# Optimization experiments

Hardware: AMD Instinct MI355X
Metric: run time of the kernel (lower is better)

The kernel has to match this reference:

```python
import jax, jax.numpy as jnp
import numpy as np

N_NODES = 100000
N_EDGES = 1250000
NUM_RELS = 8
D_IN, D_HID, D_OUT = 64, 64, 32


def setup_inputs() -> dict:
    key = jax.random.key(0)
    ks = jax.random.split(key, 10)
    x = jax.random.normal(ks[0], (N_NODES, D_IN), dtype=jnp.float32)
    src = jax.random.randint(ks[1], (N_EDGES,), 0, N_NODES, dtype=jnp.int32)
    dst = jax.random.randint(ks[2], (N_EDGES,), 0, N_NODES, dtype=jnp.int32)
    edge_type = jax.random.randint(ks[3], (N_EDGES,), 0, NUM_RELS, dtype=jnp.int32)
    s1 = 1.0 / np.sqrt(D_IN)
    s2 = 1.0 / np.sqrt(D_HID)
    W1 = jax.random.uniform(ks[4], (NUM_RELS, D_IN, D_HID), jnp.float32, -s1, s1)
    root1 = jax.random.uniform(ks[5], (D_IN, D_HID), jnp.float32, -s1, s1)
    b1 = jnp.zeros((D_HID,), jnp.float32)
    W2 = jax.random.uniform(ks[6], (NUM_RELS, D_HID, D_OUT), jnp.float32, -s2, s2)
    root2 = jax.random.uniform(ks[7], (D_HID, D_OUT), jnp.float32, -s2, s2)
    b2 = jnp.zeros((D_OUT,), jnp.float32)
    return {"x": x, "W1": W1, "root1": root1, "b1": b1,
            "W2": W2, "root2": root2, "b2": b2,
            "src": src, "dst": dst, "edge_type": edge_type}


def rgcn_conv(x, W, root, b, src, dst, edge_type, num_rels, num_nodes):
    # self-loop (root) transform + bias
    out = x @ root + b
    for r in range(num_rels):  # loop over small fixed relation set
        mask = (edge_type == r).astype(x.dtype)          # (E,)
        h = x @ W[r]                                      # (N, dout): transform once per relation
        msg = h[src] * mask[:, None]                      # (E, dout) gather + mask
        agg = jax.ops.segment_sum(msg, dst, num_segments=num_nodes)
        cnt = jax.ops.segment_sum(mask, dst, num_segments=num_nodes)
        out = out + agg / jnp.maximum(cnt, 1.0)[:, None]  # per-relation mean (PyG default aggr)
    return out


def reference(x, W1, root1, b1, W2, root2, b2, src, dst, edge_type):
    h = jax.nn.relu(rgcn_conv(x, W1, root1, b1, src, dst, edge_type, NUM_RELS, N_NODES))
    return rgcn_conv(h, W2, root2, b2, src, dst, edge_type, NUM_RELS, N_NODES)
```

## Files before the change

kernel.cpp:

```cpp
#include <hip/hip_runtime.h>

typedef _Float16 half8 __attribute__((ext_vector_type(8)));
typedef __attribute__((ext_vector_type(4))) float f32x4;

__device__ __forceinline__ unsigned short f2h(float f) {
    _Float16 h = (_Float16)f;
    return *(unsigned short*)&h;
}
__device__ __forceinline__ float h2f(unsigned short u) {
    _Float16 h = *(_Float16*)&u;
    return (float)h;
}


__device__ __forceinline__ void wprep_body(
    const float* __restrict__ W, const float* __restrict__ root,
    unsigned short* __restrict__ wb, int dout, int idx)
{
    int c = idx / (64 * dout);
    int rme = idx % (64 * dout);
    int kk = rme / dout;
    int j = rme % dout;
    float f = (c == 0) ? root[kk * dout + j]
                       : W[(size_t)(c - 1) * 64 * dout + kk * dout + j];
    wb[(size_t)c * dout * 72 + (size_t)j * 72 + kk] = f2h(f);
}

__global__ __launch_bounds__(256) void prep_kernel(
    const float* __restrict__ x, unsigned short* __restrict__ xh, int n8,
    const float* __restrict__ W1, const float* __restrict__ root1,
    unsigned short* __restrict__ wb1,
    const float* __restrict__ W2, const float* __restrict__ root2,
    unsigned short* __restrict__ wb2,
    int* __restrict__ hist, int nhist4)
{
    int id = blockIdx.x * 256 + threadIdx.x;
    if (id < n8) {
        const f32x4* p = (const f32x4*)(x + (size_t)id * 8);
        f32x4 u = p[0], v = p[1];
        half8 o;
#pragma unroll
        for (int j = 0; j < 4; ++j) {
            o[j] = (_Float16)u[j];
            o[j + 4] = (_Float16)v[j];
        }
        *(half8*)(xh + (size_t)id * 8) = o;
        return;
    }
    id -= n8;
    if (id < 9 * 64 * 64) { wprep_body(W1, root1, wb1, 64, id); return; }
    id -= 9 * 64 * 64;
    if (id < 9 * 64 * 32) { wprep_body(W2, root2, wb2, 32, id); return; }
    id -= 9 * 64 * 32;
    if (id < nhist4) ((int4*)hist)[id] = make_int4(0, 0, 0, 0);
}


__global__ __launch_bounds__(256) void hist8_kernel(
    const int* __restrict__ dst, const int* __restrict__ et,
    int* __restrict__ hist, int* __restrict__ rank, int E)
{
    int e = blockIdx.x * 256 + threadIdx.x;
    if (e < E) rank[e] = atomicAdd(&hist[dst[e] * 8 + et[e]], 1);
}

#define SCAN_TILE 4096
__global__ __launch_bounds__(1024) void scanA_kernel(
    const int* __restrict__ hist, int* __restrict__ bstart,
    int* __restrict__ partial, int nkeys)
{
    __shared__ int wsum[16];
    const int t = threadIdx.x;
    const int lane = t & 63, w = t >> 6;
    const int base = blockIdx.x * SCAN_TILE + t * 4;
    int v[4];
    int s = 0;
#pragma unroll
    for (int i = 0; i < 4; ++i) {
        v[i] = (base + i < nkeys) ? hist[base + i] : 0;
        s += v[i];
    }
    int inc = s;
#pragma unroll
    for (int off = 1; off < 64; off <<= 1) {
        int u = __shfl_up(inc, off);
        if (lane >= off) inc += u;
    }
    if (lane == 63) wsum[w] = inc;
    __syncthreads();
    if (w == 0 && lane < 16) {
        int ws = wsum[lane];
        int winc = ws;
#pragma unroll
        for (int off = 1; off < 16; off <<= 1) {
            int u = __shfl_up(winc, off);
            if (lane >= off) winc += u;
        }
        wsum[lane] = winc - ws;
    }
    __syncthreads();
    int run = wsum[w] + (inc - s);
#pragma unroll
    for (int i = 0; i < 4; ++i) {
        if (base + i < nkeys) bstart[base + i] = run;
        run += v[i];
    }
    if (t == 1023) partial[blockIdx.x] = run;
}

__global__ __launch_bounds__(64) void scanB_kernel(
    const int* __restrict__ partial, int* __restrict__ pscan,
    int* __restrict__ bstart_end, int nblk)
{
    const int lane = threadIdx.x;
    int running = 0;
    for (int b = 0; b < nblk; b += 64) {
        int i = b + lane;
        int o = (i < nblk) ? partial[i] : 0;
        int v = o;
#pragma unroll
        for (int off = 1; off < 64; off <<= 1) {
            int u = __shfl_up(v, off);
            if (lane >= off) v += u;
        }
        if (i < nblk) pscan[i] = running + v - o;
        running += __shfl(v, 63);
    }
    if (lane == 0) *bstart_end = running;
}

__global__ __launch_bounds__(256) void scatter_kernel(
    const int* __restrict__ src, const int* __restrict__ dst,
    const int* __restrict__ et, const int* __restrict__ rank,
    const int* __restrict__ bstart, const int* __restrict__ pscan,
    unsigned* __restrict__ srt, int E)
{
    int e = blockIdx.x * 256 + threadIdx.x;
    if (e < E) {
        int key = dst[e] * 8 + et[e];
        srt[bstart[key] + pscan[key >> 12] + rank[e]] = (unsigned)src[e];
    }
}


template <int DOUT, int RELU, int OUTH>
__global__ __launch_bounds__(256, 6) void fused_kernel(
    const unsigned short* __restrict__ tab,
    const unsigned* __restrict__ srt,
    const int* __restrict__ bstart,
    const int* __restrict__ pscan,
    const unsigned short* __restrict__ wb,
    const float* __restrict__ bias,
    float* __restrict__ outf,
    unsigned short* __restrict__ outh,
    int n_nodes, int Etot)
{
    __shared__ __align__(16) unsigned short Atile[16 * 600];

    const int t = threadIdx.x;
    const int w = t >> 6, lane = t & 63;
    const int quad = lane >> 4, l16 = lane & 15;
    const int nbt = blockIdx.x * 16;
    const int nb4 = nbt + w * 4;
    const int KEYS = n_nodes * 8;

    {
        const int nb0 = nb4 * 8;
        int idx = nb0 + lane; if (idx > KEYS) idx = KEYS;
        int lv;
        if (idx < KEYS) lv = bstart[idx] + pscan[idx >> 12];
        else            lv = Etot;
        const int E0 = __builtin_amdgcn_readlane(lv, 0);
        const int E1 = __builtin_amdgcn_readlane(lv, 32);

        int cntv = __shfl_down(lv, 1) - lv;
        float rsc = 1.0f / fmaxf((float)cntv, 1.0f);

#pragma unroll
        for (int i = 0; i < 4; ++i) {
            int node = nb4 + i;
            unsigned short v = 0;
            if (node < n_nodes) v = tab[(size_t)node * 64 + lane];
            Atile[(w * 4 + i) * 600 + lane] = v;
        }

        float acc0 = 0.f, acc1 = 0.f;
        int R = 0;
        int bnext = __builtin_amdgcn_readlane(lv, 1);

        auto flushes = [&](int eabs) {
            while (R < 32 && eabs == bnext) {
                float sc = __uint_as_float(
                    __builtin_amdgcn_readlane(__float_as_uint(rsc), R));
                Atile[(w * 4 + (R >> 3)) * 600 + 64 + (R & 7) * 64 + lane] =
                    f2h((acc0 + acc1) * sc);
                acc0 = 0.f; acc1 = 0.f;
                ++R;
                bnext = (R < 31) ? __builtin_amdgcn_readlane(lv, R + 1) : E1;
            }
        };

        const char* tabc = (const char*)tab;
        const unsigned loff = (unsigned)(lane << 1);
        unsigned short GA[16], GB[16];

        int base = E0;
        unsigned rec = 0;
        if (base < E1 && lane < E1 - base) rec = srt[base + lane];
        while (base < E1) {
            const int blen = min(64, E1 - base);
            const int nbase = base + 64;
            unsigned recn = 0;
            if (nbase < E1 && lane < E1 - nbase) recn = srt[nbase + lane];

#pragma unroll
            for (int i = 0; i < 16; ++i) {
                unsigned q = (unsigned)__builtin_amdgcn_readlane((int)rec, i);
                GA[i] = *(const unsigned short*)(tabc + ((size_t)q << 7) + loff);
            }
            for (int b = 0; b < blen; b += 16) {
                if (b + 16 < blen) {
#pragma unroll
                    for (int i = 0; i < 16; ++i) {
                        unsigned q = (unsigned)__builtin_amdgcn_readlane(
                            (int)rec, b + 16 + i);
                        GB[i] = *(const unsigned short*)(
                            tabc + ((size_t)q << 7) + loff);
                    }
                }
                if (b + 16 <= blen) {
#pragma unroll
                    for (int i = 0; i < 16; ++i) {
                        flushes(base + b + i);
                        if (i & 1) acc1 += h2f(GA[i]);
                        else       acc0 += h2f(GA[i]);
                    }
                } else {
#pragma unroll
                    for (int i = 0; i < 16; ++i) {
                        if (b + i < blen) {
                            flushes(base + b + i);
                            if (i & 1) acc1 += h2f(GA[i]);
                            else       acc0 += h2f(GA[i]);
                        }
                    }
                }
                if (b + 16 < blen) {
#pragma unroll
                    for (int i = 0; i < 16; ++i) GA[i] = GB[i];
                }
            }
            base = nbase; rec = recn;
        }
        flushes(E1);
        while (R < 32) {
            float sc = __uint_as_float(
                __builtin_amdgcn_readlane(__float_as_uint(rsc), R));
            Atile[(w * 4 + (R >> 3)) * 600 + 64 + (R & 7) * 64 + lane] =
                f2h((acc0 + acc1) * sc);
            acc0 = 0.f; acc1 = 0.f;
            ++R;
        }
    }

    __syncthreads();

    constexpr int JPW = DOUT / 16;
    if (JPW == 2 && w >= 2) return;

    const int j = w * 16 + l16;
    f32x4 d = {0.f, 0.f, 0.f, 0.f};
    const unsigned short* arow = &Atile[l16 * 600];
#pragma unroll
    for (int c = 0; c < 9; ++c) {
        half8 a0 = *(const half8*)(arow + c * 64 + quad * 8);
        half8 a1 = *(const half8*)(arow + c * 64 + 32 + quad * 8);
        half8 b0 = *(const half8*)&wb[c * DOUT * 72 + j * 72 + quad * 8];
        half8 b1 = *(const half8*)&wb[c * DOUT * 72 + j * 72 + 32 + quad * 8];
        d = __builtin_amdgcn_mfma_f32_16x16x32_f16(a0, b0, d, 0, 0, 0);
        d = __builtin_amdgcn_mfma_f32_16x16x32_f16(a1, b1, d, 0, 0, 0);
    }

    const float bj = bias[j];
#pragma unroll
    for (int r = 0; r < 4; ++r) {
        const int node = nbt + quad * 4 + r;
        if (node < n_nodes) {
            float v = d[r] + bj;
            if (RELU) v = fmaxf(v, 0.0f);
            if (OUTH) outh[(size_t)node * 64 + j] = f2h(v);
            else      outf[(size_t)node * DOUT + j] = v;
        }
    }
}

extern "C" void kernel_launch(void* const* d_in, const int* in_sizes, int n_in,
                              void* d_out, int out_size, void* d_ws, size_t ws_size,
                              hipStream_t stream) {
    const float* x     = (const float*)d_in[0];
    const float* W1    = (const float*)d_in[1];
    const float* root1 = (const float*)d_in[2];
    const float* b1    = (const float*)d_in[3];
    const float* W2    = (const float*)d_in[4];
    const float* root2 = (const float*)d_in[5];
    const float* b2    = (const float*)d_in[6];
    const int*   src   = (const int*)d_in[7];
    const int*   dst   = (const int*)d_in[8];
    const int*   et    = (const int*)d_in[9];

    const int N = in_sizes[0] / 64;
    const int E = in_sizes[7];
    const int KEYS = N * 8;

    char* p = (char*)d_ws;
    auto alloc = [&](size_t bytes) {
        char* r = p;
        p += (bytes + 15) & ~(size_t)15;
        return r;
    };
    unsigned* srt       = (unsigned*)alloc((size_t)E * 4);
    int* rank           = (int*)alloc((size_t)E * 4);
    int* hist           = (int*)alloc((size_t)KEYS * 4);
    int* bstart         = (int*)alloc((size_t)(KEYS + 1) * 4);
    int* partial        = (int*)alloc(256 * 4);
    int* pscan          = (int*)alloc(256 * 4);
    unsigned short* wb1 = (unsigned short*)alloc((size_t)9 * 64 * 72 * 2);
    unsigned short* wb2 = (unsigned short*)alloc((size_t)9 * 32 * 72 * 2);
    unsigned short* xh  = (unsigned short*)alloc((size_t)N * 64 * 2);
    unsigned short* h   = (unsigned short*)alloc((size_t)N * 64 * 2);

    const int n8 = N * 8;
    const int nhist4 = KEYS / 4;
    const int prep_items = n8 + 9 * 64 * 64 + 9 * 64 * 32 + nhist4;
    prep_kernel<<<(prep_items + 255) / 256, 256, 0, stream>>>(
        x, xh, n8, W1, root1, wb1, W2, root2, wb2, hist, nhist4);

    hist8_kernel<<<(E + 255) / 256, 256, 0, stream>>>(dst, et, hist, rank, E);
    const int nscan = (KEYS + SCAN_TILE - 1) / SCAN_TILE;
    scanA_kernel<<<nscan, 1024, 0, stream>>>(hist, bstart, partial, KEYS);
    scanB_kernel<<<1, 64, 0, stream>>>(partial, pscan, bstart + KEYS, nscan);
    scatter_kernel<<<(E + 255) / 256, 256, 0, stream>>>(
        src, dst, et, rank, bstart, pscan, srt, E);

    fused_kernel<64, 1, 1><<<(N + 15) / 16, 256, 0, stream>>>(
        xh, srt, bstart, pscan, wb1, b1, nullptr, h, N, E);
    fused_kernel<32, 0, 0><<<(N + 15) / 16, 256, 0, stream>>>(
        h, srt, bstart, pscan, wb2, b2, (float*)d_out, nullptr, N, E);
}
```

Baseline: 315.2 us.

## Hand-schedule gather loads with inline asm and drop rank array via atomicSub

The fused kernel's per-row gather loop is rewritten with inline-asm global_load_ushort/dword and explicit s_waitcnt vmcnt(16) double buffering across four 16-edge chunks. This keeps more gathers in flight and stops the compiler from serializing or reordering them. Separately, the per-edge rank array is removed: the scatter kernel now recovers slot positions by atomically decrementing the histogram, which saves one E-sized write and read. In exchange the order of edges within a bucket becomes nondeterministic, so float summation order can vary from run to run, and the scatter kernel takes on contended atomics.

```diff
diff --git a/kernel.cpp b/kernel.cpp
--- a/kernel.cpp
+++ b/kernel.cpp
@@ -58,10 +58,10 @@
 
 __global__ __launch_bounds__(256) void hist8_kernel(
     const int* __restrict__ dst, const int* __restrict__ et,
-    int* __restrict__ hist, int* __restrict__ rank, int E)
+    int* __restrict__ hist, int E)
 {
     int e = blockIdx.x * 256 + threadIdx.x;
-    if (e < E) rank[e] = atomicAdd(&hist[dst[e] * 8 + et[e]], 1);
+    if (e < E) atomicAdd(&hist[dst[e] * 8 + et[e]], 1);
 }
 
 #define SCAN_TILE 4096
@@ -131,14 +131,15 @@
 
 __global__ __launch_bounds__(256) void scatter_kernel(
     const int* __restrict__ src, const int* __restrict__ dst,
-    const int* __restrict__ et, const int* __restrict__ rank,
+    const int* __restrict__ et, int* __restrict__ hist,
     const int* __restrict__ bstart, const int* __restrict__ pscan,
     unsigned* __restrict__ srt, int E)
 {
     int e = blockIdx.x * 256 + threadIdx.x;
     if (e < E) {
         int key = dst[e] * 8 + et[e];
-        srt[bstart[key] + pscan[key >> 12] + rank[e]] = (unsigned)src[e];
+        int r = atomicSub(&hist[key], 1) - 1;
+        srt[bstart[key] + pscan[key >> 12] + r] = (unsigned)src[e];
     }
 }
 
@@ -201,8 +202,36 @@
         };
 
         const char* tabc = (const char*)tab;
-        const unsigned loff = (unsigned)(lane << 1);
-        unsigned short GA[16], GB[16];
+        const unsigned voff = (unsigned)(lane << 1);
+        unsigned GA[16], GB[16];
+
+#define ISSUE16(BUF, RECV, KB)                                              \
+        _Pragma("unroll")                                                   \
+        for (int i_ = 0; i_ < 16; ++i_) {                                   \
+            int q_ = __builtin_amdgcn_readlane((int)(RECV), (KB) + i_);     \
+            const char* ap_ = tabc + ((size_t)(unsigned)q_ << 7);           \
+            asm volatile("global_load_ushort %0, %1, %2"                    \
+                         : "=v"(BUF[i_]) : "v"(voff), "s"(ap_));            \
+        }
+#define WAIT16  asm volatile("s_waitcnt vmcnt(16)" ::: "memory")
+#define WAIT0   asm volatile("s_waitcnt vmcnt(0)" ::: "memory")
+#define SB      __builtin_amdgcn_sched_barrier(0)
+#define CONSUME_FULL(BUF, B)                                                \
+        _Pragma("unroll")                                                   \
+        for (int i_ = 0; i_ < 16; ++i_) {                                   \
+            flushes(base + (B) + i_);                                       \
+            if (i_ & 1) acc1 += h2f((unsigned short)BUF[i_]);               \
+            else        acc0 += h2f((unsigned short)BUF[i_]);               \
+        }
+#define CONSUME_TAIL(BUF, B)                                                \
+        _Pragma("unroll")                                                   \
+        for (int i_ = 0; i_ < 16; ++i_) {                                   \
+            if ((B) + i_ < blen) {                                          \
+                flushes(base + (B) + i_);                                   \
+                if (i_ & 1) acc1 += h2f((unsigned short)BUF[i_]);           \
+                else        acc0 += h2f((unsigned short)BUF[i_]);           \
+            }                                                               \
+        }
 
         int base = E0;
         unsigned rec = 0;
@@ -211,47 +240,43 @@
             const int blen = min(64, E1 - base);
             const int nbase = base + 64;
             unsigned recn = 0;
-            if (nbase < E1 && lane < E1 - nbase) recn = srt[nbase + lane];
-
-#pragma unroll
-            for (int i = 0; i < 16; ++i) {
-                unsigned q = (unsigned)__builtin_amdgcn_readlane((int)rec, i);
-                GA[i] = *(const unsigned short*)(tabc + ((size_t)q << 7) + loff);
-            }
-            for (int b = 0; b < blen; b += 16) {
-                if (b + 16 < blen) {
-#pragma unroll
-                    for (int i = 0; i < 16; ++i) {
-                        unsigned q = (unsigned)__builtin_amdgcn_readlane(
-                            (int)rec, b + 16 + i);
-                        GB[i] = *(const unsigned short*)(
-                            tabc + ((size_t)q << 7) + loff);
-                    }
-                }
-                if (b + 16 <= blen) {
-#pragma unroll
-                    for (int i = 0; i < 16; ++i) {
-                        flushes(base + b + i);
-                        if (i & 1) acc1 += h2f(GA[i]);
-                        else       acc0 += h2f(GA[i]);
-                    }
-                } else {
-#pragma unroll
-                    for (int i = 0; i < 16; ++i) {
-                        if (b + i < blen) {
-                            flushes(base + b + i);
-                            if (i & 1) acc1 += h2f(GA[i]);
-                            else       acc0 += h2f(GA[i]);
-                        }
-                    }
-                }
-                if (b + 16 < blen) {
-#pragma unroll
-                    for (int i = 0; i < 16; ++i) GA[i] = GB[i];
-                }
-            }
-            base = nbase; rec = recn;
-        }
+            if (nbase < E1) {
+                int ei = nbase + lane;
+                if (ei > E1 - 1) ei = E1 - 1;
+                unsigned eoff = (unsigned)ei << 2;
+                asm volatile("global_load_dword %0, %1, %2"
+                             : "=v"(recn) : "v"(eoff), "s"(srt));
+            }
+
+            const bool m1 = blen > 16, m2 = blen > 32, m3 = blen > 48;
+            ISSUE16(GA, rec, 0);
+            if (m1) { ISSUE16(GB, rec, 16); WAIT16; } else WAIT0;
+            SB;
+            if (blen >= 16) { CONSUME_FULL(GA, 0); } else { CONSUME_TAIL(GA, 0); }
+            if (m1) {
+                if (m2) { ISSUE16(GA, rec, 32); WAIT16; } else WAIT0;
+                SB;
+                if (blen >= 32) { CONSUME_FULL(GB, 16); } else { CONSUME_TAIL(GB, 16); }
+            }
+            if (m2) {
+                if (m3) { ISSUE16(GB, rec, 48); WAIT16; } else WAIT0;
+                SB;
+                if (blen >= 48) { CONSUME_FULL(GA, 32); } else { CONSUME_TAIL(GA, 32); }
+            }
+            if (m3) {
+                WAIT0;
+                SB;
+                if (blen >= 64) { CONSUME_FULL(GB, 48); } else { CONSUME_TAIL(GB, 48); }
+            }
+            base = nbase;
+            rec = recn;
+        }
+#undef ISSUE16
+#undef WAIT16
+#undef WAIT0
+#undef SB
+#undef CONSUME_FULL
+#undef CONSUME_TAIL
         flushes(E1);
         while (R < 32) {
             float sc = __uint_as_float(
@@ -319,7 +344,6 @@
         return r;
     };
     unsigned* srt       = (unsigned*)alloc((size_t)E * 4);
-    int* rank           = (int*)alloc((size_t)E * 4);
     int* hist           = (int*)alloc((size_t)KEYS * 4);
     int* bstart         = (int*)alloc((size_t)(KEYS + 1) * 4);
     int* partial        = (int*)alloc(256 * 4);
@@ -335,12 +359,12 @@
     prep_kernel<<<(prep_items + 255) / 256, 256, 0, stream>>>(
         x, xh, n8, W1, root1, wb1, W2, root2, wb2, hist, nhist4);
 
-    hist8_kernel<<<(E + 255) / 256, 256, 0, stream>>>(dst, et, hist, rank, E);
+    hist8_kernel<<<(E + 255) / 256, 256, 0, stream>>>(dst, et, hist, E);
     const int nscan = (KEYS + SCAN_TILE - 1) / SCAN_TILE;
     scanA_kernel<<<nscan, 1024, 0, stream>>>(hist, bstart, partial, KEYS);
     scanB_kernel<<<1, 64, 0, stream>>>(partial, pscan, bstart + KEYS, nscan);
     scatter_kernel<<<(E + 255) / 256, 256, 0, stream>>>(
-        src, dst, et, rank, bstart, pscan, srt, E);
+        src, dst, et, hist, bstart, pscan, srt, E);
 
     fused_kernel<64, 1, 1><<<(N + 15) / 16, 256, 0, stream>>>(
         xh, srt, bstart, pscan, wb1, b1, nullptr, h, N, E);
```

After: 354.7 us. 12.5% more time.
